# Kernel optimization log

Measured on AMD Instinct MI355X. Metric: run time of the kernel, lower is better.

The kernel has to match this reference:

```python
import jax, jax.numpy as jnp
import numpy as np

D_MODEL = 2048
D_LATENT = 512
NUM_HEADS = 16
B, T = 2, 2048


def setup_inputs() -> dict:
    key = jax.random.key(0)
    ks = jax.random.split(key, 6)
    s = 0.02  # init scale
    return {
        "x": jax.random.normal(ks[0], (B, T, D_MODEL), jnp.float32),
        # weights stored as [in, out] so y = x @ W (== torch x @ weight.T)
        "w_dkv": jax.random.normal(ks[1], (D_MODEL, D_LATENT), jnp.float32) * s,
        # w_uk kept in torch weight layout [d_model, d_latent] for absorption
        "w_uk": jax.random.normal(ks[2], (D_MODEL, D_LATENT), jnp.float32) * s,
        "w_uv": jax.random.normal(ks[3], (D_LATENT, D_MODEL), jnp.float32) * s,
        "w_q": jax.random.normal(ks[4], (D_MODEL, D_MODEL), jnp.float32) * s,
        "w_o": jax.random.normal(ks[5], (D_MODEL, D_MODEL), jnp.float32) * s,
    }


def reference(x, w_dkv, w_uk, w_uv, w_q, w_o):
    # Eval-mode MLA with weight absorption (w_q_w_uk), dropout is a no-op.
    Bsz, Tl, C = x.shape
    H = NUM_HEADS
    S = C // H
    L = w_dkv.shape[1]
    scale = 1.0 / jnp.sqrt(jnp.asarray(C, x.dtype))

    kv_latent = x @ w_dkv  # [B,T,L]

    # absorbed projection: w_q.T.view(C,H,S) einsum w_uk.view(H,S,L) -> [H,C,L]
    absorbed = jnp.einsum('chs,hsl->hcl', w_q.reshape(C, H, S), w_uk.reshape(H, S, L))

    q_lat = jnp.einsum('btc,hcl->bhtl', x, absorbed)            # [B,H,T,L]
    att = jnp.einsum('bhtl,bsl->bhts', q_lat, kv_latent) * scale  # [B,H,T,T]

    causal_mask = jnp.triu(jnp.ones((Tl, Tl), bool), k=1)
    att = jnp.where(causal_mask, jnp.asarray(-jnp.inf, att.dtype), att)
    att = jax.nn.softmax(att, axis=-1)

    v = (kv_latent @ w_uv).reshape(Bsz, Tl, H, S)               # [B,T,H,S]
    y = jnp.einsum('bhts,bshd->bthd', att, v).reshape(Bsz, Tl, C)
    return y @ w_o
```

## Files before the change

kernel.cpp:

```cpp
#include <hip/hip_runtime.h>
#include <hip/hip_bf16.h>

#define T_SEQ 2048
#define C_DIM 2048
#define L_DIM 512
#define H_NUM 16
#define S_DIM 128
#define B_SZ  2

typedef __attribute__((ext_vector_type(8))) short bf16x8;
typedef __attribute__((ext_vector_type(4))) float f32x4;
typedef __attribute__((ext_vector_type(4))) short short4v;

__device__ inline short f2bf(float f) {
    union { float f; unsigned u; } x; x.f = f;
    unsigned r = x.u + 0x7fffu + ((x.u >> 16) & 1u);
    return (short)(r >> 16);
}

__device__ __forceinline__ void tcast_body(const float* __restrict__ in, short* __restrict__ out,
                                           int R, int C, int bx, int by, int tid) {
    int c = bx * 32 + (tid & 31);
    int r = by * 8 + (tid >> 5);
    out[(long)c * R + r] = f2bf(in[(long)r * C + c]);
}

__global__ __launch_bounds__(256) void prep_kernel(
    const float* __restrict__ x, short* __restrict__ xb,
    const float* __restrict__ wq, short* __restrict__ wqT,
    const float* __restrict__ wdkv, short* __restrict__ wdkvT,
    const float* __restrict__ wuk, short* __restrict__ wukT,
    const float* __restrict__ wuv, short* __restrict__ wuvT,
    const float* __restrict__ wo, short* __restrict__ woT)
{
    int bid = blockIdx.x, tid = threadIdx.x;
    if (bid < 8192) {
        int i = bid * 256 + tid;
        float4 v = ((const float4*)x)[i];
        short4v o;
        o[0] = f2bf(v.x); o[1] = f2bf(v.y); o[2] = f2bf(v.z); o[3] = f2bf(v.w);
        ((short4v*)xb)[i] = o;
        return;
    }
    int t = bid - 8192;
    if (t < 16384)       tcast_body(wq,   wqT,   2048, 2048, t % 64,           t / 64,           tid);
    else if (t < 20480)  tcast_body(wdkv, wdkvT, 2048, 512,  (t - 16384) % 16, (t - 16384) / 16, tid);
    else if (t < 24576)  tcast_body(wuk,  wukT,  2048, 512,  (t - 20480) % 16, (t - 20480) / 16, tid);
    else if (t < 28672)  tcast_body(wuv,  wuvT,  512,  2048, (t - 24576) % 64, (t - 24576) / 64, tid);
    else                 tcast_body(wo,   woT,   2048, 2048, (t - 28672) % 64, (t - 28672) / 64, tid);
}

__global__ __launch_bounds__(256) void vtrans_kernel(const short* __restrict__ v,
                                                     short* __restrict__ vt) {
    long idx = (long)blockIdx.x * 256 + threadIdx.x;
    int t = (int)(idx & (T_SEQ - 1));
    long r = idx >> 11;
    int s = (int)(r & (S_DIM - 1)); r >>= 7;
    int h = (int)(r & (H_NUM - 1));
    int b = (int)(r >> 4);
    vt[idx] = v[((long)(b * T_SEQ + t)) * C_DIM + h * S_DIM + s];
}

__device__ __forceinline__ void gemm_body(
    const short* __restrict__ A, const short* __restrict__ Bt,
    float* __restrict__ Cf, short* __restrict__ Cb,
    int K, int lda, int ldb, int ldc, int m0, int n0, long coff, bool outf32,
    short (&As)[2][128 * 32], short (&Bs)[2][128 * 32])
{
    int tid = threadIdx.x;
    int wave = tid >> 6, l = tid & 63;
    int wm = (wave >> 1) * 64, wn = (wave & 1) * 64;
    int lr = l & 15, lhi = l >> 4;
    f32x4 acc[4][4] = {};

#define STAGE_AB(KI, BUF) do { \
        _Pragma("unroll") \
        for (int r = 0; r < 2; r++) { \
            int e = (r * 256 + tid) * 8; \
            int row = e >> 5, col = e & 31; \
            __builtin_amdgcn_global_load_lds( \
                (const __attribute__((address_space(1))) unsigned int*)(A + (long)(m0 + row) * lda + (KI) * 32 + col), \
                (__attribute__((address_space(3))) unsigned int*)(&As[BUF][e]), 16, 0, 0); \
            __builtin_amdgcn_global_load_lds( \
                (const __attribute__((address_space(1))) unsigned int*)(Bt + (long)(n0 + row) * ldb + (KI) * 32 + col), \
                (__attribute__((address_space(3))) unsigned int*)(&Bs[BUF][e]), 16, 0, 0); \
        } \
    } while (0)

    int nk = K >> 5;
    STAGE_AB(0, 0);

    for (int i = 0; i < nk; i++) {
        int cur = i & 1;
        asm volatile("s_waitcnt lgkmcnt(0)" ::: "memory");
        __builtin_amdgcn_s_barrier();
        if (i + 1 < nk) {
            STAGE_AB(i + 1, cur ^ 1);
            asm volatile("s_waitcnt vmcnt(4)" ::: "memory");
        } else {
            asm volatile("s_waitcnt vmcnt(0)" ::: "memory");
        }
        __builtin_amdgcn_s_barrier();

        bf16x8 af[4], bfr[4];
        #pragma unroll
        for (int mt = 0; mt < 4; mt++)
            af[mt] = *(const bf16x8*)&As[cur][(wm + mt * 16 + lr) * 32 + lhi * 8];
        #pragma unroll
        for (int nt = 0; nt < 4; nt++)
            bfr[nt] = *(const bf16x8*)&Bs[cur][(wn + nt * 16 + lr) * 32 + lhi * 8];
        #pragma unroll
        for (int mt = 0; mt < 4; mt++)
            #pragma unroll
            for (int nt = 0; nt < 4; nt++)
                acc[mt][nt] = __builtin_amdgcn_mfma_f32_16x16x32_bf16(af[mt], bfr[nt], acc[mt][nt], 0, 0, 0);
    }
#undef STAGE_AB

    #pragma unroll
    for (int mt = 0; mt < 4; mt++) {
        #pragma unroll
        for (int i = 0; i < 4; i++) {
            int row = m0 + wm + mt * 16 + lhi * 4 + i;
            long base = coff + (long)row * ldc + n0 + wn;
            #pragma unroll
            for (int nt = 0; nt < 4; nt++) {
                float val = acc[mt][nt][i];
                int colo = nt * 16 + lr;
                if (outf32) Cf[base + colo] = val;
                else        Cb[base + colo] = f2bf(val);
            }
        }
    }
}

__global__ __launch_bounds__(256) void gemm_bt_kernel(
    const short* __restrict__ A, const short* __restrict__ Bt, float* __restrict__ Cf,
    int K, int lda, int ldb, int ldc)
{
    __shared__ __align__(16) short As[2][128 * 32];
    __shared__ __align__(16) short Bs[2][128 * 32];
    int m0 = blockIdx.y * 128, n0 = blockIdx.x * 128;
    gemm_body(A, Bt, Cf, nullptr, K, lda, ldb, ldc, m0, n0, 0, true, As, Bs);
}

__global__ __launch_bounds__(256) void gemm2_kernel(
    const short* A0, const short* Bt0, short* Cb0, int K0, int lda0, int ldb0, int ldc0,
    long sAz0, long sBz0, long sCz0, int nx0, int nxy0, int nblk0,
    const short* A1, const short* Bt1, short* Cb1, int K1, int lda1, int ldb1, int ldc1,
    long sAz1, long sBz1, long sCz1, int nx1, int nxy1)
{
    __shared__ __align__(16) short As[2][128 * 32];
    __shared__ __align__(16) short Bs[2][128 * 32];
    int id = blockIdx.x;
    const short *A, *Bt; short* Cb; int K, lda, ldb, ldc, nx, nxy, local;
    long sAz, sBz, sCz;
    if (id < nblk0) {
        A = A0; Bt = Bt0; Cb = Cb0; K = K0; lda = lda0; ldb = ldb0; ldc = ldc0;
        sAz = sAz0; sBz = sBz0; sCz = sCz0; nx = nx0; nxy = nxy0; local = id;
    } else {
        A = A1; Bt = Bt1; Cb = Cb1; K = K1; lda = lda1; ldb = ldb1; ldc = ldc1;
        sAz = sAz1; sBz = sBz1; sCz = sCz1; nx = nx1; nxy = nxy1; local = id - nblk0;
    }
    int z = local / nxy, rem = local % nxy;
    int n0 = (rem % nx) * 128, m0 = (rem / nx) * 128;
    A += (long)z * sAz; Bt += (long)z * sBz;
    gemm_body(A, Bt, nullptr, Cb, K, lda, ldb, ldc, m0, n0, (long)z * sCz, false, As, Bs);
}

__global__ __launch_bounds__(256) void flash13_kernel(
    const short* __restrict__ qlat,
    const short* __restrict__ kv,
    const short* __restrict__ vt,
    short* __restrict__ y)
{
    __shared__ __align__(16) short Ks[32 * 512];
    __shared__ __align__(16) short Ps[4 * 16 * 32];

    int f = blockIdx.x;
    int xcd = f & 7, slot = f >> 3;
    int b = xcd >> 2;
    int h = (xcd & 3) | ((slot >> 4) << 2);
    int pr = slot & 15;
    int tid = threadIdx.x;
    int w = tid >> 6, l = tid & 63, lr = l & 15, lhi = l >> 4;
    const short* qb  = qlat + ((long)(h * B_SZ + b)) * T_SEQ * L_DIM;
    const short* kvb = kv + (long)b * T_SEQ * L_DIM;
    const short* vtb = vt + ((long)(b * H_NUM + h)) * S_DIM * T_SEQ;
    char* Pwb = (char*)(Ps + w * 512);
    const float scale = 0.022097086912079608f;

#define STAGE_K(S0ROW) do { \
        _Pragma("unroll") \
        for (int r = 0; r < 8; r++) { \
            int flat = r * 4096 + tid * 16; \
            int row = flat >> 10, colb = flat & 1023; \
            int src = (((S0ROW) + row) << 10) + (colb ^ ((row & 15) << 4)); \
            __builtin_amdgcn_global_load_lds( \
                (const __attribute__((address_space(1))) unsigned int*)((const char*)kvb + src), \
                (__attribute__((address_space(3))) unsigned int*)((char*)Ks + flat), 16, 0, 0); \
        } \
    } while (0)

    #pragma unroll 1
    for (int sel = 0; sel < 2; sel++) {
        int qt = sel ? pr : (31 - pr);
        int t0 = qt * 64;
        int wt0 = t0 + w * 16;
        int myq = wt0 + lr;

        bf16x8 qf[16];
        #pragma unroll
        for (int ks = 0; ks < 16; ks++)
            qf[ks] = *(const bf16x8*)&qb[(long)(wt0 + lr) * L_DIM + ks * 32 + lhi * 8];

        f32x4 yacc[8] = {};
        float mrun = -__builtin_inff(), lrun = 0.f;

        int nchunk = (t0 >> 5) + 2;

        if (sel == 0) STAGE_K(0);

        for (int c = 0; c < nchunk; c++) {
            int s0 = c * 32;
            asm volatile("s_waitcnt vmcnt(0)" ::: "memory");
            __builtin_amdgcn_s_barrier();

            bool active = (s0 < wt0 + 16);
            bf16x8 vf[8];
            f32x4 sc[2];
            if (active) {
                #pragma unroll
                for (int st = 0; st < 8; st++)
                    vf[st] = *(const bf16x8*)&vtb[(long)(st * 16 + lr) * T_SEQ + s0 + lhi * 8];

                #pragma unroll
                for (int ct = 0; ct < 2; ct++) {
                    int swz = lr << 4;
                    const char* kbase = (const char*)Ks + ((ct * 16 + lr) << 10);
                    f32x4 sA = {}, sB = {};
                    #pragma unroll
                    for (int ks = 0; ks < 8; ks++) {
                        bf16x8 kfA = *(const bf16x8*)(kbase + ((ks * 64 + lhi * 16) ^ swz));
                        bf16x8 kfB = *(const bf16x8*)(kbase + (((ks + 8) * 64 + lhi * 16) ^ swz));
                        sA = __builtin_amdgcn_mfma_f32_16x16x32_bf16(kfA, qf[ks], sA, 0, 0, 0);
                        sB = __builtin_amdgcn_mfma_f32_16x16x32_bf16(kfB, qf[ks + 8], sB, 0, 0, 0);
                    }
                    sc[ct] = sA + sB;
                }
            }
            asm volatile("s_waitcnt lgkmcnt(0)" ::: "memory");
            __builtin_amdgcn_s_barrier();
            if (c + 1 < nchunk) STAGE_K(s0 + 32);

            if (active) {
                float p[2][4], mx = -__builtin_inff();
                #pragma unroll
                for (int sub = 0; sub < 2; sub++)
                    #pragma unroll
                    for (int i = 0; i < 4; i++) {
                        float a = sc[sub][i] * scale;
                        int kpos = s0 + sub * 16 + lhi * 4 + i;
                        if (kpos > myq) a = -__builtin_inff();
                        p[sub][i] = a;
                        mx = fmaxf(mx, a);
                    }
                mx = fmaxf(mx, __shfl_xor(mx, 16));
                mx = fmaxf(mx, __shfl_xor(mx, 32));

                unsigned long long grew = __ballot(mx > mrun);
                if (grew) {
                    float mnew = fmaxf(mrun, mx);
                    float fac = __expf(mrun - mnew);
                    mrun = mnew;
                    lrun *= fac;
                    float facr[4];
                    #pragma unroll
                    for (int i = 0; i < 4; i++)
                        facr[i] = __shfl(fac, lhi * 4 + i);
                    #pragma unroll
                    for (int st = 0; st < 8; st++)
                        #pragma unroll
                        for (int i = 0; i < 4; i++)
                            yacc[st][i] *= facr[i];
                }
                float ls = 0.f;
                #pragma unroll
                for (int sub = 0; sub < 2; sub++)
                    #pragma unroll
                    for (int i = 0; i < 4; i++) {
                        p[sub][i] = __expf(p[sub][i] - mrun);
                        ls += p[sub][i];
                    }
                ls += __shfl_xor(ls, 16);
                ls += __shfl_xor(ls, 32);
                lrun += ls;

                int swz = (lr & 3) << 4;
                char* pb = Pwb + lr * 64;
                #pragma unroll
                for (int sub = 0; sub < 2; sub++) {
                    short4v pk;
                    #pragma unroll
                    for (int i = 0; i < 4; i++) pk[i] = f2bf(p[sub][i]);
                    *(short4v*)(pb + ((sub * 32 + lhi * 8) ^ swz)) = pk;
                }
                asm volatile("s_waitcnt lgkmcnt(0)" ::: "memory");
                __builtin_amdgcn_sched_barrier(0);
                bf16x8 pf = *(const bf16x8*)(Pwb + lr * 64 + ((lhi * 16) ^ swz));
                #pragma unroll
                for (int st = 0; st < 8; st++)
                    yacc[st] = __builtin_amdgcn_mfma_f32_16x16x32_bf16(pf, vf[st], yacc[st], 0, 0, 0);
            }
        }

        if (sel == 0) STAGE_K(0);

        float lrunr[4];
        #pragma unroll
        for (int i = 0; i < 4; i++)
            lrunr[i] = __shfl(lrun, lhi * 4 + i);
        #pragma unroll
        for (int st = 0; st < 8; st++)
            #pragma unroll
            for (int i = 0; i < 4; i++) {
                int trow = wt0 + lhi * 4 + i;
                float val = yacc[st][i] / lrunr[i];
                y[((long)(b * T_SEQ + trow)) * C_DIM + h * S_DIM + st * 16 + lr] = f2bf(val);
            }
    }
#undef STAGE_K
}

extern "C" void kernel_launch(void* const* d_in, const int* in_sizes, int n_in,
                              void* d_out, int out_size, void* d_ws, size_t ws_size,
                              hipStream_t stream) {
    const float* x    = (const float*)d_in[0];
    const float* wdkv = (const float*)d_in[1];
    const float* wuk  = (const float*)d_in[2];
    const float* wuv  = (const float*)d_in[3];
    const float* wq   = (const float*)d_in[4];
    const float* wo   = (const float*)d_in[5];
    float* out = (float*)d_out;

    short* ws = (short*)d_ws;
    size_t off = 0;
    short* xb    = ws + off; off += (size_t)4096 * 2048;
    short* wqT   = ws + off; off += (size_t)2048 * 2048;
    short* wdkvT = ws + off; off += (size_t)512 * 2048;
    short* wukT  = ws + off; off += (size_t)512 * 2048;
    short* wuvT  = ws + off; off += (size_t)2048 * 512;
    short* woT   = ws + off; off += (size_t)2048 * 2048;
    short* q     = ws + off; off += (size_t)4096 * 2048;
    short* kvb   = ws + off; off += (size_t)4096 * 512;
    short* vbuf  = ws + off; off += (size_t)4096 * 2048;
    short* qlat  = ws + off; off += (size_t)H_NUM * B_SZ * T_SEQ * L_DIM;
    short* vtb  = xb;
    short* ybuf = q;

    prep_kernel<<<53248, 256, 0, stream>>>(x, xb, wq, wqT, wdkv, wdkvT,
                                           wuk, wukT, wuv, wuvT, wo, woT);

    gemm2_kernel<<<640, 256, 0, stream>>>(
        xb, wqT, q, 2048, 2048, 2048, 2048, 0, 0, 0, 16, 512, 512,
        xb, wdkvT, kvb, 2048, 2048, 2048, 512, 0, 0, 0, 4, 128);

    gemm2_kernel<<<2560, 256, 0, stream>>>(
        kvb, wuvT, vbuf, 512, 512, 512, 2048, 0, 0, 0, 16, 512, 512,
        q, wukT, qlat, 128, 2048, 2048, 512, 128, 128, (long)B_SZ * T_SEQ * L_DIM, 4, 128);

    vtrans_kernel<<<32768, 256, 0, stream>>>(vbuf, vtb);
    flash13_kernel<<<dim3(512, 1, 1), 256, 0, stream>>>(qlat, kvb, vtb, ybuf);
    gemm_bt_kernel<<<dim3(16, 32, 1), 256, 0, stream>>>(ybuf, woT, out, 2048, 2048, 2048, 2048);
}
```

Before: 397.2 us.

## Tile weight and V transposes through LDS, fold softmax scale into q-latent GEMM

The element-wise weight transpose-casts and the V transpose are replaced by 64x64 tiles staged in shared memory, so global reads and writes become vectorised and coalesced. This sharply reduces the block count of the prep and vtrans launches. The softmax scale times log2(e) is folded into the q-latent GEMM epilogue, and the attention loop switches to exp2f and only applies the causal mask on diagonal chunks. Scaling before the bf16 rounding of q_lat slightly changes numerics.

After: 357.6 us. 1.11x faster.

```diff
diff --git a/kernel.cpp b/kernel.cpp
--- a/kernel.cpp
+++ b/kernel.cpp
@@ -18,11 +18,27 @@
     return (short)(r >> 16);
 }
 
-__device__ __forceinline__ void tcast_body(const float* __restrict__ in, short* __restrict__ out,
-                                           int R, int C, int bx, int by, int tid) {
-    int c = bx * 32 + (tid & 31);
-    int r = by * 8 + (tid >> 5);
-    out[(long)c * R + r] = f2bf(in[(long)r * C + c]);
+__device__ __forceinline__ void wtile_body(const float* __restrict__ in, short* __restrict__ out,
+                                           int R, int C, int r0, int c0, int tid) {
+    __shared__ float lds[64][66];
+    #pragma unroll
+    for (int it = 0; it < 4; it++) {
+        int r = (tid >> 4) + it * 16;
+        int c4 = (tid & 15) * 4;
+        float4 v = *(const float4*)&in[(long)(r0 + r) * C + c0 + c4];
+        lds[c4 + 0][r] = v.x; lds[c4 + 1][r] = v.y;
+        lds[c4 + 2][r] = v.z; lds[c4 + 3][r] = v.w;
+    }
+    __syncthreads();
+    #pragma unroll
+    for (int it = 0; it < 4; it++) {
+        int c = tid >> 2;
+        int rb = (tid & 3) * 16 + it * 4;
+        short4v o;
+        #pragma unroll
+        for (int j = 0; j < 4; j++) o[j] = f2bf(lds[c][rb + j]);
+        *(short4v*)&out[(long)(c0 + c) * R + r0 + rb] = o;
+    }
 }
 
 __global__ __launch_bounds__(256) void prep_kernel(
@@ -43,28 +59,44 @@
         return;
     }
     int t = bid - 8192;
-    if (t < 16384)       tcast_body(wq,   wqT,   2048, 2048, t % 64,           t / 64,           tid);
-    else if (t < 20480)  tcast_body(wdkv, wdkvT, 2048, 512,  (t - 16384) % 16, (t - 16384) / 16, tid);
-    else if (t < 24576)  tcast_body(wuk,  wukT,  2048, 512,  (t - 20480) % 16, (t - 20480) / 16, tid);
-    else if (t < 28672)  tcast_body(wuv,  wuvT,  512,  2048, (t - 24576) % 64, (t - 24576) / 64, tid);
-    else                 tcast_body(wo,   woT,   2048, 2048, (t - 28672) % 64, (t - 28672) / 64, tid);
+    if (t < 1024)       wtile_body(wq,   wqT,   2048, 2048, (t >> 5) * 64,            (t & 31) * 64, tid);
+    else if (t < 1280)  wtile_body(wdkv, wdkvT, 2048, 512,  ((t - 1024) >> 3) * 64,   ((t - 1024) & 7) * 64, tid);
+    else if (t < 1536)  wtile_body(wuk,  wukT,  2048, 512,  ((t - 1280) >> 3) * 64,   ((t - 1280) & 7) * 64, tid);
+    else if (t < 1792)  wtile_body(wuv,  wuvT,  512,  2048, ((t - 1536) >> 5) * 64,   ((t - 1536) & 31) * 64, tid);
+    else                wtile_body(wo,   woT,   2048, 2048, ((t - 1792) >> 5) * 64,   ((t - 1792) & 31) * 64, tid);
 }
 
 __global__ __launch_bounds__(256) void vtrans_kernel(const short* __restrict__ v,
                                                      short* __restrict__ vt) {
-    long idx = (long)blockIdx.x * 256 + threadIdx.x;
-    int t = (int)(idx & (T_SEQ - 1));
-    long r = idx >> 11;
-    int s = (int)(r & (S_DIM - 1)); r >>= 7;
-    int h = (int)(r & (H_NUM - 1));
-    int b = (int)(r >> 4);
-    vt[idx] = v[((long)(b * T_SEQ + t)) * C_DIM + h * S_DIM + s];
+    __shared__ short lds[64][68];
+    int id = blockIdx.x;
+    int b = id >> 10, t2 = id & 1023;
+    int t0 = (t2 >> 5) * 64, c0 = (t2 & 31) * 64;
+    const short* in = v + (long)b * T_SEQ * C_DIM;
+    short* out = vt + (long)b * T_SEQ * C_DIM;
+    int tid = threadIdx.x;
+    #pragma unroll
+    for (int it = 0; it < 4; it++) {
+        int t = (tid >> 4) + it * 16;
+        int c4 = (tid & 15) * 4;
+        short4v vv = *(const short4v*)&in[(long)(t0 + t) * C_DIM + c0 + c4];
+        lds[c4 + 0][t] = vv[0]; lds[c4 + 1][t] = vv[1];
+        lds[c4 + 2][t] = vv[2]; lds[c4 + 3][t] = vv[3];
+    }
+    __syncthreads();
+    #pragma unroll
+    for (int it = 0; it < 4; it++) {
+        int c = tid >> 2;
+        int tb = (tid & 3) * 16 + it * 4;
+        short4v o = *(const short4v*)&lds[c][tb];
+        *(short4v*)&out[(long)(c0 + c) * C_DIM + t0 + tb] = o;
+    }
 }
 
 __device__ __forceinline__ void gemm_body(
     const short* __restrict__ A, const short* __restrict__ Bt,
     float* __restrict__ Cf, short* __restrict__ Cb,
-    int K, int lda, int ldb, int ldc, int m0, int n0, long coff, bool outf32,
+    int K, int lda, int ldb, int ldc, int m0, int n0, long coff, bool outf32, float cscale,
     short (&As)[2][128 * 32], short (&Bs)[2][128 * 32])
 {
     int tid = threadIdx.x;
@@ -125,7 +157,7 @@
             long base = coff + (long)row * ldc + n0 + wn;
             #pragma unroll
             for (int nt = 0; nt < 4; nt++) {
-                float val = acc[mt][nt][i];
+                float val = acc[mt][nt][i] * cscale;
                 int colo = nt * 16 + lr;
                 if (outf32) Cf[base + colo] = val;
                 else        Cb[base + colo] = f2bf(val);
@@ -141,31 +173,31 @@
     __shared__ __align__(16) short As[2][128 * 32];
     __shared__ __align__(16) short Bs[2][128 * 32];
     int m0 = blockIdx.y * 128, n0 = blockIdx.x * 128;
-    gemm_body(A, Bt, Cf, nullptr, K, lda, ldb, ldc, m0, n0, 0, true, As, Bs);
+    gemm_body(A, Bt, Cf, nullptr, K, lda, ldb, ldc, m0, n0, 0, true, 1.0f, As, Bs);
 }
 
 __global__ __launch_bounds__(256) void gemm2_kernel(
     const short* A0, const short* Bt0, short* Cb0, int K0, int lda0, int ldb0, int ldc0,
-    long sAz0, long sBz0, long sCz0, int nx0, int nxy0, int nblk0,
+    long sAz0, long sBz0, long sCz0, int nx0, int nxy0, int nblk0, float cscale0,
     const short* A1, const short* Bt1, short* Cb1, int K1, int lda1, int ldb1, int ldc1,
-    long sAz1, long sBz1, long sCz1, int nx1, int nxy1)
+    long sAz1, long sBz1, long sCz1, int nx1, int nxy1, float cscale1)
 {
     __shared__ __align__(16) short As[2][128 * 32];
     __shared__ __align__(16) short Bs[2][128 * 32];
     int id = blockIdx.x;
     const short *A, *Bt; short* Cb; int K, lda, ldb, ldc, nx, nxy, local;
-    long sAz, sBz, sCz;
+    long sAz, sBz, sCz; float cs;
     if (id < nblk0) {
         A = A0; Bt = Bt0; Cb = Cb0; K = K0; lda = lda0; ldb = ldb0; ldc = ldc0;
-        sAz = sAz0; sBz = sBz0; sCz = sCz0; nx = nx0; nxy = nxy0; local = id;
+        sAz = sAz0; sBz = sBz0; sCz = sCz0; nx = nx0; nxy = nxy0; local = id; cs = cscale0;
     } else {
         A = A1; Bt = Bt1; Cb = Cb1; K = K1; lda = lda1; ldb = ldb1; ldc = ldc1;
-        sAz = sAz1; sBz = sBz1; sCz = sCz1; nx = nx1; nxy = nxy1; local = id - nblk0;
+        sAz = sAz1; sBz = sBz1; sCz = sCz1; nx = nx1; nxy = nxy1; local = id - nblk0; cs = cscale1;
     }
     int z = local / nxy, rem = local % nxy;
     int n0 = (rem % nx) * 128, m0 = (rem / nx) * 128;
     A += (long)z * sAz; Bt += (long)z * sBz;
-    gemm_body(A, Bt, nullptr, Cb, K, lda, ldb, ldc, m0, n0, (long)z * sCz, false, As, Bs);
+    gemm_body(A, Bt, nullptr, Cb, K, lda, ldb, ldc, m0, n0, (long)z * sCz, false, cs, As, Bs);
 }
 
 __global__ __launch_bounds__(256) void flash13_kernel(
@@ -188,7 +220,6 @@
     const short* kvb = kv + (long)b * T_SEQ * L_DIM;
     const short* vtb = vt + ((long)(b * H_NUM + h)) * S_DIM * T_SEQ;
     char* Pwb = (char*)(Ps + w * 512);
-    const float scale = 0.022097086912079608f;
 
 #define STAGE_K(S0ROW) do { \
         _Pragma("unroll") \
@@ -254,24 +285,34 @@
             if (c + 1 < nchunk) STAGE_K(s0 + 32);
 
             if (active) {
-                float p[2][4], mx = -__builtin_inff();
+                float p[2][4];
                 #pragma unroll
                 for (int sub = 0; sub < 2; sub++)
                     #pragma unroll
-                    for (int i = 0; i < 4; i++) {
-                        float a = sc[sub][i] * scale;
-                        int kpos = s0 + sub * 16 + lhi * 4 + i;
-                        if (kpos > myq) a = -__builtin_inff();
-                        p[sub][i] = a;
-                        mx = fmaxf(mx, a);
-                    }
+                    for (int i = 0; i < 4; i++)
+                        p[sub][i] = sc[sub][i];
+                if (s0 + 31 > wt0) {
+                    #pragma unroll
+                    for (int sub = 0; sub < 2; sub++)
+                        #pragma unroll
+                        for (int i = 0; i < 4; i++) {
+                            int kpos = s0 + sub * 16 + lhi * 4 + i;
+                            if (kpos > myq) p[sub][i] = -__builtin_inff();
+                        }
+                }
+                float mx = -__builtin_inff();
+                #pragma unroll
+                for (int sub = 0; sub < 2; sub++)
+                    #pragma unroll
+                    for (int i = 0; i < 4; i++)
+                        mx = fmaxf(mx, p[sub][i]);
                 mx = fmaxf(mx, __shfl_xor(mx, 16));
                 mx = fmaxf(mx, __shfl_xor(mx, 32));
 
                 unsigned long long grew = __ballot(mx > mrun);
                 if (grew) {
                     float mnew = fmaxf(mrun, mx);
-                    float fac = __expf(mrun - mnew);
+                    float fac = exp2f(mrun - mnew);
                     mrun = mnew;
                     lrun *= fac;
                     float facr[4];
@@ -289,7 +330,7 @@
                 for (int sub = 0; sub < 2; sub++)
                     #pragma unroll
                     for (int i = 0; i < 4; i++) {
-                        p[sub][i] = __expf(p[sub][i] - mrun);
+                        p[sub][i] = exp2f(p[sub][i] - mrun);
                         ls += p[sub][i];
                     }
                 ls += __shfl_xor(ls, 16);
@@ -358,18 +399,20 @@
     short* vtb  = xb;
     short* ybuf = q;
 
-    prep_kernel<<<53248, 256, 0, stream>>>(x, xb, wq, wqT, wdkv, wdkvT,
+    const float qscale = 0.022097086912079608f * 1.4426950408889634f;
+
+    prep_kernel<<<11008, 256, 0, stream>>>(x, xb, wq, wqT, wdkv, wdkvT,
                                            wuk, wukT, wuv, wuvT, wo, woT);
 
     gemm2_kernel<<<640, 256, 0, stream>>>(
-        xb, wqT, q, 2048, 2048, 2048, 2048, 0, 0, 0, 16, 512, 512,
-        xb, wdkvT, kvb, 2048, 2048, 2048, 512, 0, 0, 0, 4, 128);
+        xb, wqT, q, 2048, 2048, 2048, 2048, 0, 0, 0, 16, 512, 512, 1.0f,
+        xb, wdkvT, kvb, 2048, 2048, 2048, 512, 0, 0, 0, 4, 128, 1.0f);
 
     gemm2_kernel<<<2560, 256, 0, stream>>>(
-        kvb, wuvT, vbuf, 512, 512, 512, 2048, 0, 0, 0, 16, 512, 512,
-        q, wukT, qlat, 128, 2048, 2048, 512, 128, 128, (long)B_SZ * T_SEQ * L_DIM, 4, 128);
-
-    vtrans_kernel<<<32768, 256, 0, stream>>>(vbuf, vtb);
+        kvb, wuvT, vbuf, 512, 512, 512, 2048, 0, 0, 0, 16, 512, 512, 1.0f,
+        q, wukT, qlat, 128, 2048, 2048, 512, 128, 128, (long)B_SZ * T_SEQ * L_DIM, 4, 128, qscale);
+
+    vtrans_kernel<<<2048, 256, 0, stream>>>(vbuf, vtb);
     flash13_kernel<<<dim3(512, 1, 1), 256, 0, stream>>>(qlat, kvb, vtb, ybuf);
     gemm_bt_kernel<<<dim3(16, 32, 1), 256, 0, stream>>>(ybuf, woT, out, 2048, 2048, 2048, 2048);
 }
```
